# Kernel optimization log

Hardware: AMD Instinct MI355X
Metric: run time of the kernel (lower is better)

## Reference

```python
import jax, jax.numpy as jnp
import numpy as np

B, T, D = 2, 2048, 2048
H, L = 16, 64
Hd = D // H  # 128
SCALE = 1.0 / np.sqrt(L).astype(np.float32)


def apply_rope(q, k, freqs):
    # q, k: [B, T, H, Hd]; freqs: [T, Hd//2] angles (theta)
    cos = jnp.cos(freqs)[None, :, None, :]  # [1,T,1,Hd/2]
    sin = jnp.sin(freqs)[None, :, None, :]

    def rot(t):
        tr = t.reshape(*t.shape[:-1], Hd // 2, 2)
        a, b = tr[..., 0], tr[..., 1]
        return jnp.stack([a * cos - b * sin, a * sin + b * cos], axis=-1).reshape(t.shape)

    return rot(q), rot(k)


def setup_inputs() -> dict:
    key = jax.random.key(0)
    ks = jax.random.split(key, 16)

    def w(k, shape):
        return jax.random.normal(k, shape, jnp.float32) * 0.02

    x = jax.random.normal(ks[0], (B, T, D), jnp.float32)
    # RoPE angles: theta[t, i] = t / 10000^(2i/Hd)
    inv = 1.0 / (10000.0 ** (jnp.arange(0, Hd, 2, dtype=jnp.float32) / Hd))
    freqs = jnp.arange(T, dtype=jnp.float32)[:, None] * inv[None, :]  # [T, Hd/2]
    # additive causal mask
    mask = jnp.where(jnp.tril(jnp.ones((T, T), bool)), 0.0, -1e9).astype(jnp.float32)

    return dict(
        x=x, freqs=freqs, mask=mask,
        Wq=w(ks[1], (D, D)), bq=jnp.zeros((D,), jnp.float32),
        Wk=w(ks[2], (D, D)), bk=jnp.zeros((D,), jnp.float32),
        Wv=w(ks[3], (D, D)), bv=jnp.zeros((D,), jnp.float32),
        Wo=w(ks[4], (D, D)), bo=jnp.zeros((D,), jnp.float32),
        Wcq=w(ks[5], (Hd, L)), bcq=jnp.zeros((L,), jnp.float32),
        Wck=w(ks[6], (Hd, L)), bck=jnp.zeros((L,), jnp.float32),
        Wcv=w(ks[7], (Hd, L)), bcv=jnp.zeros((L,), jnp.float32),
        Wd=w(ks[8], (L, Hd)), bd=jnp.zeros((Hd,), jnp.float32),
    )


def reference(x, freqs, mask, Wq, bq, Wk, bk, Wv, bv, Wo, bo,
              Wcq, bcq, Wck, bck, Wcv, bcv, Wd, bd):
    b, t, d = x.shape
    q = (x @ Wq + bq).reshape(b, t, H, Hd)
    k = (x @ Wk + bk).reshape(b, t, H, Hd)
    v = (x @ Wv + bv).reshape(b, t, H, Hd)

    q, k = apply_rope(q, k, freqs)

    # per-head latent compression [B,T,H,L]
    q_lat = jnp.einsum('bthd,dl->bthl', q, Wcq) + bcq
    k_lat = jnp.einsum('bthd,dl->bthl', k, Wck) + bck
    v_lat = jnp.einsum('bthd,dl->bthl', v, Wcv) + bcv

    scores = jnp.einsum('bthl,bshl->bhts', q_lat, k_lat) * SCALE
    scores = scores + mask[None, None, :, :]
    attn = jax.nn.softmax(scores, axis=-1)

    out = jnp.einsum('bhts,bshl->bthl', attn, v_lat)  # [B,T,H,L]
    out = jnp.einsum('bthl,lk->bthk', out, Wd) + bd    # decompress -> [B,T,H,Hd]
    out = out.reshape(b, t, d)
    return out @ Wo + bo
```

## Files before the change

kernel.cpp:

```cpp
#include <hip/hip_runtime.h>
#include <hip/hip_bf16.h>

static constexpr int Bsz = 2;
static constexpr int Tn  = 2048;
static constexpr int Dn  = 2048;
static constexpr int Hn  = 16;
static constexpr int Ln  = 64;
static constexpr int Hd  = 128;
static constexpr float SL2E = 0.125f * 1.44269504088896f;

typedef short short8 __attribute__((ext_vector_type(8)));
typedef float f32x4 __attribute__((ext_vector_type(4)));
typedef unsigned short ushort8 __attribute__((ext_vector_type(8)));
typedef unsigned short ushort4v __attribute__((ext_vector_type(4)));
typedef _Float16 half8 __attribute__((ext_vector_type(8)));
typedef unsigned short u16;

__device__ inline u16 f16_rne(float f) {
  _Float16 h = (_Float16)f;
  union { _Float16 h; u16 u; } x; x.h = h;
  return x.u;
}
__device__ inline float f16_to_f(u16 u) {
  union { u16 u; _Float16 h; } x; x.u = u;
  return (float)x.h;
}

#define GL(g, l) __builtin_amdgcn_global_load_lds(                     \
    (const __attribute__((address_space(1))) void*)(g),                \
    (__attribute__((address_space(3))) void*)(l), 16, 0, 0)

__global__ void split_h(const float* __restrict__ A, u16* __restrict__ O,
                        int nblk, int Kd) {
  int b = blockIdx.x * 256 + threadIdx.x;
  if (b >= nblk) return;
  int perRow = Kd >> 3;
  int m = b / perRow, gb = b - m * perRow;
  int w = gb >> 2, g = gb & 3;
  const float* src = A + (size_t)m * Kd + (w << 5) + (g << 2);
  float4 v0 = *(const float4*)src;
  float4 v1 = *(const float4*)(src + 16);
  float e[8] = {v0.x, v0.y, v0.z, v0.w, v1.x, v1.y, v1.z, v1.w};
  ushort8 o;
#pragma unroll
  for (int j = 0; j < 8; ++j) o[j] = f16_rne(e[j]);
  *(ushort8*)(O + (size_t)b * 8) = o;
}

__global__ __launch_bounds__(256) void transpose_h(
    const float* __restrict__ W, u16* __restrict__ Th, int Kd, int Nd) {
  __shared__ float t[32][33];
  int k0 = blockIdx.x * 32, n0 = blockIdx.y * 32;
  int i = threadIdx.x;
  {
    int kk = i >> 3, nn = (i & 7) << 2;
    float4 v = *(const float4*)&W[(size_t)(k0 + kk) * Nd + n0 + nn];
    t[kk][nn] = v.x; t[kk][nn + 1] = v.y; t[kk][nn + 2] = v.z; t[kk][nn + 3] = v.w;
  }
  __syncthreads();
  int n = i >> 3, t2 = i & 7;
  int g = t2 >> 1, h = t2 & 1;
  int kbase = h * 16 + g * 4;
  ushort4v o;
#pragma unroll
  for (int j = 0; j < 4; ++j) o[j] = f16_rne(t[kbase + j][n]);
  *(ushort4v*)(Th + (size_t)(n0 + n) * Kd + k0 + t2 * 4) = o;
}

__global__ __launch_bounds__(256) void fold64(
    const float* __restrict__ A, int lda, int a_bx, int a_by,
    const float* __restrict__ B, int ldb, int b_bx, int b_by,
    float* __restrict__ C, int ldc, int c_bx, int c_by) {
  __shared__ float a_lds[64][132];
  __shared__ float b_lds[128][64];
  const int bx = blockIdx.x, by = blockIdx.y, tid = threadIdx.x;
  A += (size_t)bx * a_bx + (size_t)by * a_by;
  B += (size_t)bx * b_bx + (size_t)by * b_by;
  C += (size_t)bx * c_bx + (size_t)by * c_by;
  for (int i = tid; i < 64 * 32; i += 256) {
    int r = i >> 5, c4 = (i & 31) << 2;
    *(float4*)&a_lds[r][c4] = *(const float4*)&A[(size_t)r * lda + c4];
  }
  for (int i = tid; i < 128 * 16; i += 256) {
    int r = i >> 4, c4 = (i & 15) << 2;
    *(float4*)&b_lds[r][c4] = *(const float4*)&B[(size_t)r * ldb + c4];
  }
  __syncthreads();
  const int r = tid >> 2, l0 = (tid & 3) << 4;
  float acc[16] = {};
  for (int k = 0; k < 128; ++k) {
    float av = a_lds[r][k];
    const float* bp = &b_lds[k][l0];
#pragma unroll
    for (int j = 0; j < 16; ++j) acc[j] += av * bp[j];
  }
#pragma unroll
  for (int j4 = 0; j4 < 4; ++j4)
    *(float4*)&C[(size_t)r * ldc + l0 + j4 * 4] = *(float4*)&acc[j4 * 4];
}

__global__ __launch_bounds__(256) void bias_prep(
    const float* __restrict__ bv, const float* __restrict__ Wcv,
    const float* __restrict__ bcv, const float* __restrict__ bd,
    const float* __restrict__ Wo, const float* __restrict__ bo,
    float* __restrict__ bias_vf, float* __restrict__ bias_out) {
  __shared__ float red[4][64];
  if (blockIdx.x == 32) {
    for (int e = threadIdx.x; e < 1024; e += 256) {
      int h = e >> 6, l = e & 63;
      float s = bcv[l];
      for (int j = 0; j < 128; ++j) s += bv[h * 128 + j] * Wcv[j * 64 + l];
      bias_vf[e] = s;
    }
  } else {
    int n0 = blockIdx.x * 64;
    int c = threadIdx.x & 63, g = threadIdx.x >> 6;
    float s = 0.f;
    for (int k = g * 512; k < (g + 1) * 512; ++k)
      s += bd[k & 127] * Wo[(size_t)k * 2048 + n0 + c];
    red[g][c] = s;
    __syncthreads();
    if (g == 0)
      bias_out[n0 + c] = red[0][c] + red[1][c] + red[2][c] + red[3][c] + bo[n0 + c];
  }
}

__global__ __launch_bounds__(256) void gemm_qkv(
    const u16* __restrict__ Af, const u16* __restrict__ Bf,
    u16* __restrict__ cQ, u16* __restrict__ cK, u16* __restrict__ cV,
    const float* __restrict__ bq, const float* __restrict__ bk,
    const float* __restrict__ bvf, int K) {
  __shared__ u16 s[2][2][128 * 64];
  const int tid = threadIdx.x;
  const int lane = tid & 63;
  const int w = tid >> 6, wr = w >> 1, wc = w & 1;
  const int l15 = lane & 15, lg = lane >> 4;
  const int row0 = blockIdx.y * 128, col0 = blockIdx.x * 128;

  const int sr = tid >> 3, sq = tid & 7;
  const int sg = sq ^ (sr & 7);
  size_t aoff[4], boff[4];
#pragma unroll
  for (int j = 0; j < 4; ++j) {
    aoff[j] = (size_t)(row0 + j * 32 + sr) * K + sg * 8;
    boff[j] = (size_t)(col0 + j * 32 + sr) * K + sg * 8;
  }

  f32x4 acc[4][4];
#pragma unroll
  for (int i2 = 0; i2 < 4; ++i2)
#pragma unroll
    for (int j2 = 0; j2 < 4; ++j2) acc[i2][j2] = (f32x4){0.f, 0.f, 0.f, 0.f};

  int fa[4][2], fb[4][2];
#pragma unroll
  for (int mi = 0; mi < 4; ++mi) {
    int ra = wr * 64 + mi * 16 + l15;
    int rb = wc * 64 + mi * 16 + l15;
#pragma unroll
    for (int kk = 0; kk < 2; ++kk) {
      fa[mi][kk] = ra * 128 + (((kk * 4 + lg) ^ (ra & 7)) << 4);
      fb[mi][kk] = rb * 128 + (((kk * 4 + lg) ^ (rb & 7)) << 4);
    }
  }

#pragma unroll
  for (int j = 0; j < 4; ++j) {
    GL(Af + aoff[j], (char*)&s[0][0][0] + j * 4096 + tid * 16);
    GL(Bf + boff[j], (char*)&s[0][1][0] + j * 4096 + tid * 16);
  }
  int cur = 0;
  for (int k0 = 0; k0 < K; k0 += 64) {
    __syncthreads();
    if (k0 + 64 < K) {
      const int nb = cur ^ 1;
#pragma unroll
      for (int j = 0; j < 4; ++j) {
        GL(Af + aoff[j] + k0 + 64, (char*)&s[nb][0][0] + j * 4096 + tid * 16);
        GL(Bf + boff[j] + k0 + 64, (char*)&s[nb][1][0] + j * 4096 + tid * 16);
      }
    }
#pragma unroll
    for (int kk = 0; kk < 2; ++kk) {
      half8 a[4], b[4];
#pragma unroll
      for (int mi = 0; mi < 4; ++mi) {
        a[mi] = *(const half8*)((const char*)&s[cur][0][0] + fa[mi][kk]);
        b[mi] = *(const half8*)((const char*)&s[cur][1][0] + fb[mi][kk]);
      }
#pragma unroll
      for (int mi = 0; mi < 4; ++mi)
#pragma unroll
        for (int ni = 0; ni < 4; ++ni)
          acc[mi][ni] = __builtin_amdgcn_mfma_f32_16x16x32_f16(a[mi], b[ni], acc[mi][ni], 0, 0, 0);
    }
    cur ^= 1;
  }
  u16* Cp; const float* bp; int ldc, cl0;
  if (col0 < 2048)      { Cp = cQ; bp = bq;  ldc = 2048; cl0 = col0; }
  else if (col0 < 4096) { Cp = cK; bp = bk;  ldc = 2048; cl0 = col0 - 2048; }
  else                  { Cp = cV; bp = bvf; ldc = 1024; cl0 = col0 - 4096; }
#pragma unroll
  for (int ni = 0; ni < 4; ++ni) {
    int c = cl0 + wc * 64 + ni * 16 + l15;
    float bias = bp[c];
#pragma unroll
    for (int mi = 0; mi < 4; ++mi) {
      int rr = row0 + wr * 64 + mi * 16 + lg * 4;
#pragma unroll
      for (int r = 0; r < 4; ++r)
        Cp[(size_t)(rr + r) * ldc + c] = f16_rne(acc[mi][ni][r] + bias);
    }
  }
}

__global__ __launch_bounds__(256) void gemm_f16(
    const u16* __restrict__ Af, const u16* __restrict__ Bf,
    const float* __restrict__ bias, float* __restrict__ C,
    int M, int N, int K) {
  __shared__ u16 s[2][2][128 * 64];
  const int tid = threadIdx.x;
  const int lane = tid & 63;
  const int w = tid >> 6, wr = w >> 1, wc = w & 1;
  const int l15 = lane & 15, lg = lane >> 4;
  const int row0 = blockIdx.y * 128, col0 = blockIdx.x * 128;

  const int sr = tid >> 3, sq = tid & 7;
  const int sg = sq ^ (sr & 7);
  size_t aoff[4], boff[4];
#pragma unroll
  for (int j = 0; j < 4; ++j) {
    aoff[j] = (size_t)(row0 + j * 32 + sr) * K + sg * 8;
    boff[j] = (size_t)(col0 + j * 32 + sr) * K + sg * 8;
  }

  f32x4 acc[4][4];
#pragma unroll
  for (int i2 = 0; i2 < 4; ++i2)
#pragma unroll
    for (int j2 = 0; j2 < 4; ++j2) acc[i2][j2] = (f32x4){0.f, 0.f, 0.f, 0.f};

  int fa[4][2], fb[4][2];
#pragma unroll
  for (int mi = 0; mi < 4; ++mi) {
    int ra = wr * 64 + mi * 16 + l15;
    int rb = wc * 64 + mi * 16 + l15;
#pragma unroll
    for (int kk = 0; kk < 2; ++kk) {
      fa[mi][kk] = ra * 128 + (((kk * 4 + lg) ^ (ra & 7)) << 4);
      fb[mi][kk] = rb * 128 + (((kk * 4 + lg) ^ (rb & 7)) << 4);
    }
  }

#pragma unroll
  for (int j = 0; j < 4; ++j) {
    GL(Af + aoff[j], (char*)&s[0][0][0] + j * 4096 + tid * 16);
    GL(Bf + boff[j], (char*)&s[0][1][0] + j * 4096 + tid * 16);
  }
  int cur = 0;
  for (int k0 = 0; k0 < K; k0 += 64) {
    __syncthreads();
    if (k0 + 64 < K) {
      const int nb = cur ^ 1;
#pragma unroll
      for (int j = 0; j < 4; ++j) {
        GL(Af + aoff[j] + k0 + 64, (char*)&s[nb][0][0] + j * 4096 + tid * 16);
        GL(Bf + boff[j] + k0 + 64, (char*)&s[nb][1][0] + j * 4096 + tid * 16);
      }
    }
#pragma unroll
    for (int kk = 0; kk < 2; ++kk) {
      half8 a[4], b[4];
#pragma unroll
      for (int mi = 0; mi < 4; ++mi) {
        a[mi] = *(const half8*)((const char*)&s[cur][0][0] + fa[mi][kk]);
        b[mi] = *(const half8*)((const char*)&s[cur][1][0] + fb[mi][kk]);
      }
#pragma unroll
      for (int mi = 0; mi < 4; ++mi)
#pragma unroll
        for (int ni = 0; ni < 4; ++ni)
          acc[mi][ni] = __builtin_amdgcn_mfma_f32_16x16x32_f16(a[mi], b[ni], acc[mi][ni], 0, 0, 0);
    }
    cur ^= 1;
  }
#pragma unroll
  for (int ni = 0; ni < 4; ++ni) {
    int c = col0 + wc * 64 + ni * 16 + l15;
    float bv = bias[c];
#pragma unroll
    for (int mi = 0; mi < 4; ++mi) {
      int rr = row0 + wr * 64 + mi * 16 + lg * 4;
#pragma unroll
      for (int r = 0; r < 4; ++r)
        C[(size_t)(rr + r) * N + c] = acc[mi][ni][r] + bv;
    }
  }
}

__global__ __launch_bounds__(256) void compress_qk_mfma(
    const u16* __restrict__ src, const u16* __restrict__ WcT,
    const float* __restrict__ bc, const float* __restrict__ freqs,
    u16* __restrict__ dst) {
  __shared__ u16 q_lds[64 * 128];
  __shared__ u16 w_lds[64 * 128];
  const int tid = threadIdx.x;
  const int lane = tid & 63;
  const int w = tid >> 6;
  const int t0 = blockIdx.x * 64;
  const int bh = blockIdx.y, b = bh >> 4, h = bh & 15;

#pragma unroll
  for (int j = 0; j < 4; ++j) {
    int idx = tid + j * 256;
    int row = idx >> 4, slot = idx & 15;
    GL(WcT + (size_t)row * 128 + (size_t)(slot ^ (row & 7)) * 8,
       (char*)w_lds + idx * 16);
  }
  const int r = tid >> 2, seg = tid & 3;
  const u16* qp = src + ((size_t)(b * Tn + t0 + r)) * Dn + h * 128 + seg * 32;
  const float* fp = freqs + (size_t)(t0 + r) * 64 + seg * 16;
  float fr[16];
#pragma unroll
  for (int j = 0; j < 4; ++j) *(float4*)&fr[4 * j] = ((const float4*)fp)[j];
#pragma unroll
  for (int j = 0; j < 8; ++j) {
    ushort4v uv = *(const ushort4v*)(qp + 4 * j);
    float e0 = f16_to_f(uv[0]), e1 = f16_to_f(uv[1]);
    float e2 = f16_to_f(uv[2]), e3 = f16_to_f(uv[3]);
    float s0, c0, s1, c1;
    sincosf(fr[2 * j], &s0, &c0);
    sincosf(fr[2 * j + 1], &s1, &c1);
    ushort4v u;
    u[0] = f16_rne(e0 * c0 - e1 * s0);
    u[1] = f16_rne(e0 * s0 + e1 * c0);
    u[2] = f16_rne(e2 * c1 - e3 * s1);
    u[3] = f16_rne(e2 * s1 + e3 * c1);
    int slot = seg * 4 + (j & 3);
    *(ushort4v*)((char*)q_lds + r * 256 + ((slot ^ (r & 7)) << 4) + (j >> 2) * 8) = u;
  }
  __syncthreads();
  const int l15 = lane & 15, lg = lane >> 4;
  const int arow = w * 16 + l15;
  half8 af[4];
#pragma unroll
  for (int ks = 0; ks < 4; ++ks)
    af[ks] = *(const half8*)((const char*)q_lds + arow * 256 +
                             (((ks * 4 + lg) ^ (arow & 7)) << 4));
  f32x4 acc[4];
#pragma unroll
  for (int ni = 0; ni < 4; ++ni) acc[ni] = (f32x4){0.f, 0.f, 0.f, 0.f};
#pragma unroll
  for (int ni = 0; ni < 4; ++ni) {
    const int brow = ni * 16 + l15;
#pragma unroll
    for (int ks = 0; ks < 4; ++ks) {
      half8 bf = *(const half8*)((const char*)w_lds + brow * 256 +
                                 (((ks * 4 + lg) ^ (brow & 7)) << 4));
      acc[ni] = __builtin_amdgcn_mfma_f32_16x16x32_f16(af[ks], bf, acc[ni], 0, 0, 0);
    }
  }
  __syncthreads();
#pragma unroll
  for (int ni = 0; ni < 4; ++ni) {
    int lat = ni * 16 + l15;
    float bcv = bc[lat];
    int p = (lat & 32) + ((lat >> 2) & 3) * 8 + ((lat >> 4) & 1) * 4 + (lat & 3);
#pragma unroll
    for (int reg = 0; reg < 4; ++reg)
      q_lds[w * 1024 + (lg * 4 + reg) * 64 + p] = f16_rne(acc[ni][reg] + bcv);
  }
  __syncthreads();
#pragma unroll
  for (int j = 0; j < 2; ++j) {
    int idx = tid + j * 256;
    int row = idx >> 3, c8 = idx & 7;
    ushort8 val = *(const ushort8*)&q_lds[row * 64 + c8 * 8];
    *(ushort8*)(dst + ((size_t)bh * Tn + t0 + row) * 64 + c8 * 8) = val;
  }
}

__global__ __launch_bounds__(256) void transpose_v(
    const u16* __restrict__ vlat, u16* __restrict__ vlatT) {
  __shared__ u16 o_lds[64][64];
  const int tid = threadIdx.x;
  const int t0 = blockIdx.x * 64;
  const int bh = blockIdx.y, b = bh >> 4, h = bh & 15;
  const int tt = tid >> 2, lseg = tid & 3;
  const u16* vp = vlat + (size_t)(b * Tn + t0 + tt) * 1024 + h * 64 + lseg * 16;
#pragma unroll
  for (int g = 0; g < 4; ++g) {
    ushort4v u = *(const ushort4v*)(vp + g * 4);
    *(ushort4v*)&o_lds[tt][lseg * 16 + ((g ^ (tt & 3)) << 2)] = u;
  }
  __syncthreads();
  const int lat = tid >> 2, tseg = tid & 3;
  const int tw = tseg >> 1, h4 = tseg & 1;
  u16 vals[16];
#pragma unroll
  for (int i = 0; i < 16; ++i)
    vals[i] = o_lds[tseg * 16 + i][lat ^ ((i & 3) << 2)];
  u16* dp = vlatT + ((size_t)bh * 64 + lat) * Tn + t0 + tw * 32 + h4 * 4;
#pragma unroll
  for (int g = 0; g < 4; ++g) {
    ushort4v u = {vals[g * 4 + 0], vals[g * 4 + 1], vals[g * 4 + 2], vals[g * 4 + 3]};
    *(ushort4v*)(dp + g * 8) = u;
  }
}

__global__ __launch_bounds__(256) void attn_mfma(
    const u16* __restrict__ qlat, const u16* __restrict__ klat,
    const u16* __restrict__ vlatT, u16* __restrict__ oh) {
  __shared__ u16 Ks[64 * 72];
  __shared__ u16 Vs[64 * 72];
  __shared__ u16 Os[64][72];
  const int tid = threadIdx.x;
  const int lane = tid & 63;
  const int w = tid >> 6;
  const int lin = (int)(blockIdx.x + blockIdx.y * gridDim.x);
  const int nchunk = (int)(gridDim.x * gridDim.y) >> 3;
  const int swz = (lin & 7) * nchunk + (lin >> 3);
  const int bh = swz >> 5, b = bh >> 4, h = bh & 15;
  const int q0 = (31 - (swz & 31)) * 64;
  const int qw = q0 + w * 16;
  const u16* ql = qlat + (size_t)bh * Tn * 64;
  const u16* kl = klat + (size_t)bh * Tn * 64;
  const u16* vt = vlatT + (size_t)bh * 64 * Tn;
  const int l15 = lane & 15, lg = lane >> 4;

  half8 qf[2];
#pragma unroll
  for (int ks = 0; ks < 2; ++ks)
    qf[ks] = *(const half8*)(const void*)(ql + (size_t)(qw + l15) * 64 + (ks * 4 + lg) * 8);

  f32x4 accO[4];
#pragma unroll
  for (int mi = 0; mi < 4; ++mi) accO[mi] = (f32x4){0.f, 0.f, 0.f, 0.f};
  float mrow = -1e30f, lrow = 0.f;

  const int srow = tid >> 2, spair = tid & 3;
  u16* ksw = &Ks[srow * 72 + spair * 16];
  u16* vsw = &Vs[srow * 72 + spair * 16];
  const u16* kgp = kl + (size_t)srow * 64 + spair * 16;
  const u16* vgp = vt + (size_t)srow * Tn + spair * 16;

  ushort8 kr0 = *(const ushort8*)(kgp);
  ushort8 kr1 = *(const ushort8*)(kgp + 8);
  ushort8 vr0 = *(const ushort8*)(vgp);
  ushort8 vr1 = *(const ushort8*)(vgp + 8);

  const int ntiles = q0 / 64 + 1;
  for (int kt = 0; kt < ntiles; ++kt) {
    const int k0 = kt * 64;
    __syncthreads();
    *(ushort8*)ksw       = kr0;
    *(ushort8*)(ksw + 8) = kr1;
    *(ushort8*)vsw       = vr0;
    *(ushort8*)(vsw + 8) = vr1;
    __syncthreads();
    {
      int kn = k0 + 64; kn = kn > (int)Tn - 64 ? (int)Tn - 64 : kn;
      kr0 = *(const ushort8*)(kgp + (size_t)kn * 64);
      kr1 = *(const ushort8*)(kgp + (size_t)kn * 64 + 8);
      vr0 = *(const ushort8*)(vgp + kn);
      vr1 = *(const ushort8*)(vgp + kn + 8);
    }
    f32x4 s4[4];
#pragma unroll
    for (int mi = 0; mi < 4; ++mi) s4[mi] = (f32x4){0.f, 0.f, 0.f, 0.f};
    __builtin_amdgcn_s_setprio(1);
#pragma unroll
    for (int ks = 0; ks < 2; ++ks) {
      half8 kf[4];
#pragma unroll
      for (int mi = 0; mi < 4; ++mi)
        kf[mi] = *(const half8*)(const void*)&Ks[(mi * 16 + l15) * 72 + (ks * 4 + lg) * 8];
#pragma unroll
      for (int mi = 0; mi < 4; ++mi)
        s4[mi] = __builtin_amdgcn_mfma_f32_16x16x32_f16(kf[mi], qf[ks], s4[mi], 0, 0, 0);
    }
    __builtin_amdgcn_s_setprio(0);
    const bool needmask = (kt == ntiles - 1);
    const int qidx = qw + l15;
    float p[4][4];
    float tmax = -1e30f;
#pragma unroll
    for (int mi = 0; mi < 4; ++mi)
#pragma unroll
      for (int rr = 0; rr < 4; ++rr) {
        float v = s4[mi][rr] * SL2E;
        if (needmask && (k0 + mi * 16 + lg * 4 + rr > qidx)) v = -1e30f;
        p[mi][rr] = v;
        tmax = fmaxf(tmax, v);
      }
    tmax = fmaxf(tmax, __shfl_xor(tmax, 16));
    tmax = fmaxf(tmax, __shfl_xor(tmax, 32));
    if (!__all(tmax - mrow <= 8.f)) {
      float mnew = fmaxf(mrow, tmax);
      float alpha = exp2f(mrow - mnew);
      lrow *= alpha;
#pragma unroll
      for (int mi = 0; mi < 4; ++mi)
#pragma unroll
        for (int rr = 0; rr < 4; ++rr) accO[mi][rr] *= alpha;
      mrow = mnew;
    }
    float psum = 0.f;
    u16 ph[4][4];
#pragma unroll
    for (int mi = 0; mi < 4; ++mi)
#pragma unroll
      for (int rr = 0; rr < 4; ++rr) {
        float e = exp2f(p[mi][rr] - mrow);
        u16 hb = f16_rne(e);
        psum += f16_to_f(hb);
        ph[mi][rr] = hb;
      }
    psum += __shfl_xor(psum, 16);
    psum += __shfl_xor(psum, 32);
    lrow += psum;
    ushort8 pf[2];
#pragma unroll
    for (int ks = 0; ks < 2; ++ks) {
      ushort8 f;
#pragma unroll
      for (int rr = 0; rr < 4; ++rr) {
        f[rr]     = ph[2 * ks][rr];
        f[4 + rr] = ph[2 * ks + 1][rr];
      }
      pf[ks] = f;
    }
    __builtin_amdgcn_s_setprio(1);
#pragma unroll
    for (int ks = 0; ks < 2; ++ks) {
      half8 vf[4];
#pragma unroll
      for (int mi = 0; mi < 4; ++mi)
        vf[mi] = *(const half8*)(const void*)&Vs[(mi * 16 + l15) * 72 + (ks * 4 + lg) * 8];
#pragma unroll
      for (int mi = 0; mi < 4; ++mi)
        accO[mi] = __builtin_amdgcn_mfma_f32_16x16x32_f16(vf[mi], *(const half8*)&pf[ks], accO[mi], 0, 0, 0);
    }
    __builtin_amdgcn_s_setprio(0);
  }
  __syncthreads();
  {
    float inv = 1.f / lrow;
    int qloc = w * 16 + l15;
#pragma unroll
    for (int mi = 0; mi < 4; ++mi) {
      int pbase = (mi >> 1) * 32 + lg * 8 + (mi & 1) * 4;
      ushort4v u;
#pragma unroll
      for (int rr = 0; rr < 4; ++rr) u[rr] = f16_rne(accO[mi][rr] * inv);
      *(ushort4v*)&Os[qloc][pbase] = u;
    }
  }
  __syncthreads();
  {
    int rid = tid >> 2, seg = tid & 3;
    u16* dstp = oh + ((size_t)(b * Tn + q0 + rid)) * 1024 + h * 64 + seg * 16;
#pragma unroll
    for (int g = 0; g < 2; ++g)
      *(ushort8*)(dstp + g * 8) = *(const ushort8*)&Os[rid][seg * 16 + g * 8];
  }
}

extern "C" void kernel_launch(void* const* d_in, const int* in_sizes, int n_in,
                              void* d_out, int out_size, void* d_ws, size_t ws_size,
                              hipStream_t stream) {
  const float* x     = (const float*)d_in[0];
  const float* freqs = (const float*)d_in[1];
  const float* Wq  = (const float*)d_in[3];  const float* bq  = (const float*)d_in[4];
  const float* Wk  = (const float*)d_in[5];  const float* bk  = (const float*)d_in[6];
  const float* Wv  = (const float*)d_in[7];  const float* bv  = (const float*)d_in[8];
  const float* Wo  = (const float*)d_in[9];  const float* bo  = (const float*)d_in[10];
  const float* Wcq = (const float*)d_in[11]; const float* bcq = (const float*)d_in[12];
  const float* Wck = (const float*)d_in[13]; const float* bck = (const float*)d_in[14];
  const float* Wcv = (const float*)d_in[15]; const float* bcv = (const float*)d_in[16];
  const float* Wd  = (const float*)d_in[17]; const float* bd  = (const float*)d_in[18];
  float* out = (float*)d_out;

  const size_t BT = (size_t)Bsz * Tn;
  const size_t nQ = BT * Dn;
  const size_t nL = BT * Hn * Ln;
  const size_t nWT = (size_t)5120 * 2048;

  char* ws = (char*)d_ws;
  u16* xf   = (u16*)ws;
  u16* WTf  = xf + nQ;
  float* Wvf = (float*)(WTf + nWT);
  u16* Qh   = (u16*)(Wvf + (size_t)2048 * 1024);
  u16* Kh   = Qh + nQ;
  u16* vlat = Kh + nQ;
  float* bias_vf  = (float*)(vlat + (size_t)4096 * 1024);
  float* bias_out = bias_vf + 1024;
  u16* qlat  = (u16*)(bias_out + 2048);
  u16* klat  = qlat + nL;
  u16* vlatT = klat + nL;
  u16* oh = (u16*)(vlatT + nL);
  float* Wdo = (float*)(oh + (size_t)4096 * 1024);
  u16* WdoT = (u16*)(Wdo + (size_t)1024 * 2048);
  u16* WcqT = WdoT + (size_t)2048 * 1024;
  u16* WckT = WcqT + (size_t)64 * 128;

  dim3 blk(256);
  int nblkA = (int)(nQ / 8);

  split_h<<<(nblkA + 255) / 256, blk, 0, stream>>>(x, xf, nblkA, Dn);
  fold64<<<dim3(32, 16), blk, 0, stream>>>(Wv, 2048, 64 * 2048, 128,
                                           Wcv, 64, 0, 0,
                                           Wvf, 1024, 64 * 1024, 64);
  transpose_h<<<dim3(64, 64), blk, 0, stream>>>(Wq, WTf, 2048, 2048);
  transpose_h<<<dim3(64, 64), blk, 0, stream>>>(Wk, WTf + (size_t)2048 * 2048, 2048, 2048);
  transpose_h<<<dim3(64, 32), blk, 0, stream>>>(Wvf, WTf + (size_t)4096 * 2048, 2048, 1024);
  transpose_h<<<dim3(4, 2), blk, 0, stream>>>(Wcq, WcqT, 128, 64);
  transpose_h<<<dim3(4, 2), blk, 0, stream>>>(Wck, WckT, 128, 64);
  bias_prep<<<33, blk, 0, stream>>>(bv, Wcv, bcv, bd, Wo, bo, bias_vf, bias_out);

  gemm_qkv<<<dim3(40, 32), blk, 0, stream>>>(xf, WTf, Qh, Kh, vlat,
                                             bq, bk, bias_vf, 2048);

  dim3 gc(Tn / 64, Bsz * Hn);
  compress_qk_mfma<<<gc, blk, 0, stream>>>(Qh, WcqT, bcq, freqs, qlat);
  compress_qk_mfma<<<gc, blk, 0, stream>>>(Kh, WckT, bck, freqs, klat);
  transpose_v<<<gc, blk, 0, stream>>>(vlat, vlatT);

  attn_mfma<<<dim3(Tn / 64, Bsz * Hn), blk, 0, stream>>>(qlat, klat, vlatT, oh);

  fold64<<<dim3(32, 16), blk, 0, stream>>>(Wd, 128, 0, 0,
                                           Wo, 2048, 64, 128 * 2048,
                                           Wdo, 2048, 64, 64 * 2048);
  transpose_h<<<dim3(32, 64), blk, 0, stream>>>(Wdo, WdoT, 1024, 2048);
  gemm_f16<<<dim3(16, 32), blk, 0, stream>>>(oh, WdoT, bias_out, out, (int)BT, 2048, 1024);
}
```

Measured before the change: 330.9 us.

## Use 8-wave GEMM blocks, XCD tile swizzle, and batch small launches via gridDim.z

Both f16 GEMMs now run 512-thread blocks with a 2x4 wave grid, so each wave computes a 64x32 sub-tile of the same 128x128 block tile. This halves per-wave accumulators and raises the number of waves available to hide latency. gemm_qkv also remaps block indices so neighbouring tiles land on the same XCD, aiming for better L2 reuse. Separately, the Q/K weight transposes and the Q/K latent compressions are merged into single launches using blockIdx.z, cutting launch count. The trade-off is more LDS fragment reads per MFMA and a higher register and sync cost per block.

```diff
diff --git a/kernel.cpp b/kernel.cpp
--- a/kernel.cpp
+++ b/kernel.cpp
@@ -47,8 +47,11 @@
   *(ushort8*)(O + (size_t)b * 8) = o;
 }
 
-__global__ __launch_bounds__(256) void transpose_h(
-    const float* __restrict__ W, u16* __restrict__ Th, int Kd, int Nd) {
+__global__ __launch_bounds__(256) void transpose_h2(
+    const float* __restrict__ W0, const float* __restrict__ W1,
+    u16* __restrict__ T0, u16* __restrict__ T1, int Kd, int Nd) {
+  const float* W = blockIdx.z ? W1 : W0;
+  u16* Th = blockIdx.z ? T1 : T0;
   __shared__ float t[32][33];
   int k0 = blockIdx.x * 32, n0 = blockIdx.y * 32;
   int i = threadIdx.x;
@@ -125,7 +128,7 @@
   }
 }
 
-__global__ __launch_bounds__(256) void gemm_qkv(
+__global__ __launch_bounds__(512) void gemm_qkv(
     const u16* __restrict__ Af, const u16* __restrict__ Bf,
     u16* __restrict__ cQ, u16* __restrict__ cK, u16* __restrict__ cV,
     const float* __restrict__ bq, const float* __restrict__ bk,
@@ -133,41 +136,48 @@
   __shared__ u16 s[2][2][128 * 64];
   const int tid = threadIdx.x;
   const int lane = tid & 63;
-  const int w = tid >> 6, wr = w >> 1, wc = w & 1;
+  const int w = tid >> 6;
+  const int wr = w >> 2, wc = w & 3;
   const int l15 = lane & 15, lg = lane >> 4;
-  const int row0 = blockIdx.y * 128, col0 = blockIdx.x * 128;
+  const int lin = (int)(blockIdx.x + blockIdx.y * gridDim.x);
+  const int swz = (lin & 7) * 160 + (lin >> 3);
+  const int row0 = (swz / 40) * 128, col0 = (swz % 40) * 128;
 
   const int sr = tid >> 3, sq = tid & 7;
   const int sg = sq ^ (sr & 7);
-  size_t aoff[4], boff[4];
-#pragma unroll
-  for (int j = 0; j < 4; ++j) {
-    aoff[j] = (size_t)(row0 + j * 32 + sr) * K + sg * 8;
-    boff[j] = (size_t)(col0 + j * 32 + sr) * K + sg * 8;
-  }
-
-  f32x4 acc[4][4];
+  size_t aoff[2], boff[2];
+#pragma unroll
+  for (int j = 0; j < 2; ++j) {
+    aoff[j] = (size_t)(row0 + j * 64 + sr) * K + sg * 8;
+    boff[j] = (size_t)(col0 + j * 64 + sr) * K + sg * 8;
+  }
+
+  f32x4 acc[4][2];
 #pragma unroll
   for (int i2 = 0; i2 < 4; ++i2)
 #pragma unroll
-    for (int j2 = 0; j2 < 4; ++j2) acc[i2][j2] = (f32x4){0.f, 0.f, 0.f, 0.f};
-
-  int fa[4][2], fb[4][2];
+    for (int j2 = 0; j2 < 2; ++j2) acc[i2][j2] = (f32x4){0.f, 0.f, 0.f, 0.f};
+
+  int fa[4][2], fb[2][2];
 #pragma unroll
   for (int mi = 0; mi < 4; ++mi) {
     int ra = wr * 64 + mi * 16 + l15;
-    int rb = wc * 64 + mi * 16 + l15;
-#pragma unroll
-    for (int kk = 0; kk < 2; ++kk) {
+#pragma unroll
+    for (int kk = 0; kk < 2; ++kk)
       fa[mi][kk] = ra * 128 + (((kk * 4 + lg) ^ (ra & 7)) << 4);
-      fb[mi][kk] = rb * 128 + (((kk * 4 + lg) ^ (rb & 7)) << 4);
-    }
-  }
-
-#pragma unroll
-  for (int j = 0; j < 4; ++j) {
-    GL(Af + aoff[j], (char*)&s[0][0][0] + j * 4096 + tid * 16);
-    GL(Bf + boff[j], (char*)&s[0][1][0] + j * 4096 + tid * 16);
+  }
+#pragma unroll
+  for (int ni = 0; ni < 2; ++ni) {
+    int rb = wc * 32 + ni * 16 + l15;
+#pragma unroll
+    for (int kk = 0; kk < 2; ++kk)
+      fb[ni][kk] = 16384 + rb * 128 + (((kk * 4 + lg) ^ (rb & 7)) << 4);
+  }
+
+#pragma unroll
+  for (int j = 0; j < 2; ++j) {
+    GL(Af + aoff[j], (char*)&s[0][0][0] + j * 8192 + tid * 16);
+    GL(Bf + boff[j], (char*)&s[0][1][0] + j * 8192 + tid * 16);
   }
   int cur = 0;
   for (int k0 = 0; k0 < K; k0 += 64) {
@@ -175,23 +185,24 @@
     if (k0 + 64 < K) {
       const int nb = cur ^ 1;
 #pragma unroll
-      for (int j = 0; j < 4; ++j) {
-        GL(Af + aoff[j] + k0 + 64, (char*)&s[nb][0][0] + j * 4096 + tid * 16);
-        GL(Bf + boff[j] + k0 + 64, (char*)&s[nb][1][0] + j * 4096 + tid * 16);
+      for (int j = 0; j < 2; ++j) {
+        GL(Af + aoff[j] + k0 + 64, (char*)&s[nb][0][0] + j * 8192 + tid * 16);
+        GL(Bf + boff[j] + k0 + 64, (char*)&s[nb][1][0] + j * 8192 + tid * 16);
       }
     }
 #pragma unroll
     for (int kk = 0; kk < 2; ++kk) {
-      half8 a[4], b[4];
-#pragma unroll
-      for (int mi = 0; mi < 4; ++mi) {
+      half8 a[4], b[2];
+#pragma unroll
+      for (int mi = 0; mi < 4; ++mi)
         a[mi] = *(const half8*)((const char*)&s[cur][0][0] + fa[mi][kk]);
-        b[mi] = *(const half8*)((const char*)&s[cur][1][0] + fb[mi][kk]);
-      }
-#pragma unroll
-      for (int mi = 0; mi < 4; ++mi)
-#pragma unroll
-        for (int ni = 0; ni < 4; ++ni)
+#pragma unroll
+      for (int ni = 0; ni < 2; ++ni)
+        b[ni] = *(const half8*)((const char*)&s[cur][0][0] + fb[ni][kk]);
+#pragma unroll
+      for (int mi = 0; mi < 4; ++mi)
+#pragma unroll
+        for (int ni = 0; ni < 2; ++ni)
           acc[mi][ni] = __builtin_amdgcn_mfma_f32_16x16x32_f16(a[mi], b[ni], acc[mi][ni], 0, 0, 0);
     }
     cur ^= 1;
@@ -201,8 +212,8 @@
   else if (col0 < 4096) { Cp = cK; bp = bk;  ldc = 2048; cl0 = col0 - 2048; }
   else                  { Cp = cV; bp = bvf; ldc = 1024; cl0 = col0 - 4096; }
 #pragma unroll
-  for (int ni = 0; ni < 4; ++ni) {
-    int c = cl0 + wc * 64 + ni * 16 + l15;
+  for (int ni = 0; ni < 2; ++ni) {
+    int c = cl0 + wc * 32 + ni * 16 + l15;
     float bias = bp[c];
 #pragma unroll
     for (int mi = 0; mi < 4; ++mi) {
@@ -214,48 +225,53 @@
   }
 }
 
-__global__ __launch_bounds__(256) void gemm_f16(
+__global__ __launch_bounds__(512) void gemm_f16(
     const u16* __restrict__ Af, const u16* __restrict__ Bf,
     const float* __restrict__ bias, float* __restrict__ C,
     int M, int N, int K) {
   __shared__ u16 s[2][2][128 * 64];
   const int tid = threadIdx.x;
   const int lane = tid & 63;
-  const int w = tid >> 6, wr = w >> 1, wc = w & 1;
+  const int w = tid >> 6;
+  const int wr = w >> 2, wc = w & 3;
   const int l15 = lane & 15, lg = lane >> 4;
   const int row0 = blockIdx.y * 128, col0 = blockIdx.x * 128;
 
   const int sr = tid >> 3, sq = tid & 7;
   const int sg = sq ^ (sr & 7);
-  size_t aoff[4], boff[4];
-#pragma unroll
-  for (int j = 0; j < 4; ++j) {
-    aoff[j] = (size_t)(row0 + j * 32 + sr) * K + sg * 8;
-    boff[j] = (size_t)(col0 + j * 32 + sr) * K + sg * 8;
-  }
-
-  f32x4 acc[4][4];
+  size_t aoff[2], boff[2];
+#pragma unroll
+  for (int j = 0; j < 2; ++j) {
+    aoff[j] = (size_t)(row0 + j * 64 + sr) * K + sg * 8;
+    boff[j] = (size_t)(col0 + j * 64 + sr) * K + sg * 8;
+  }
+
+  f32x4 acc[4][2];
 #pragma unroll
   for (int i2 = 0; i2 < 4; ++i2)
 #pragma unroll
-    for (int j2 = 0; j2 < 4; ++j2) acc[i2][j2] = (f32x4){0.f, 0.f, 0.f, 0.f};
-
-  int fa[4][2], fb[4][2];
+    for (int j2 = 0; j2 < 2; ++j2) acc[i2][j2] = (f32x4){0.f, 0.f, 0.f, 0.f};
+
+  int fa[4][2], fb[2][2];
 #pragma unroll
   for (int mi = 0; mi < 4; ++mi) {
     int ra = wr * 64 + mi * 16 + l15;
-    int rb = wc * 64 + mi * 16 + l15;
-#pragma unroll
-    for (int kk = 0; kk < 2; ++kk) {
+#pragma unroll
+    for (int kk = 0; kk < 2; ++kk)
       fa[mi][kk] = ra * 128 + (((kk * 4 + lg) ^ (ra & 7)) << 4);
-      fb[mi][kk] = rb * 128 + (((kk * 4 + lg) ^ (rb & 7)) << 4);
-    }
-  }
-
-#pragma unroll
-  for (int j = 0; j < 4; ++j) {
-    GL(Af + aoff[j], (char*)&s[0][0][0] + j * 4096 + tid * 16);
-    GL(Bf + boff[j], (char*)&s[0][1][0] + j * 4096 + tid * 16);
+  }
+#pragma unroll
+  for (int ni = 0; ni < 2; ++ni) {
+    int rb = wc * 32 + ni * 16 + l15;
+#pragma unroll
+    for (int kk = 0; kk < 2; ++kk)
+      fb[ni][kk] = 16384 + rb * 128 + (((kk * 4 + lg) ^ (rb & 7)) << 4);
+  }
+
+#pragma unroll
+  for (int j = 0; j < 2; ++j) {
+    GL(Af + aoff[j], (char*)&s[0][0][0] + j * 8192 + tid * 16);
+    GL(Bf + boff[j], (char*)&s[0][1][0] + j * 8192 + tid * 16);
   }
   int cur = 0;
   for (int k0 = 0; k0 < K; k0 += 64) {
@@ -263,30 +279,31 @@
     if (k0 + 64 < K) {
       const int nb = cur ^ 1;
 #pragma unroll
-      for (int j = 0; j < 4; ++j) {
-        GL(Af + aoff[j] + k0 + 64, (char*)&s[nb][0][0] + j * 4096 + tid * 16);
-        GL(Bf + boff[j] + k0 + 64, (char*)&s[nb][1][0] + j * 4096 + tid * 16);
+      for (int j = 0; j < 2; ++j) {
+        GL(Af + aoff[j] + k0 + 64, (char*)&s[nb][0][0] + j * 8192 + tid * 16);
+        GL(Bf + boff[j] + k0 + 64, (char*)&s[nb][1][0] + j * 8192 + tid * 16);
       }
     }
 #pragma unroll
     for (int kk = 0; kk < 2; ++kk) {
-      half8 a[4], b[4];
-#pragma unroll
-      for (int mi = 0; mi < 4; ++mi) {
+      half8 a[4], b[2];
+#pragma unroll
+      for (int mi = 0; mi < 4; ++mi)
         a[mi] = *(const half8*)((const char*)&s[cur][0][0] + fa[mi][kk]);
-        b[mi] = *(const half8*)((const char*)&s[cur][1][0] + fb[mi][kk]);
-      }
-#pragma unroll
-      for (int mi = 0; mi < 4; ++mi)
-#pragma unroll
-        for (int ni = 0; ni < 4; ++ni)
+#pragma unroll
+      for (int ni = 0; ni < 2; ++ni)
+        b[ni] = *(const half8*)((const char*)&s[cur][0][0] + fb[ni][kk]);
+#pragma unroll
+      for (int mi = 0; mi < 4; ++mi)
+#pragma unroll
+        for (int ni = 0; ni < 2; ++ni)
           acc[mi][ni] = __builtin_amdgcn_mfma_f32_16x16x32_f16(a[mi], b[ni], acc[mi][ni], 0, 0, 0);
     }
     cur ^= 1;
   }
 #pragma unroll
-  for (int ni = 0; ni < 4; ++ni) {
-    int c = col0 + wc * 64 + ni * 16 + l15;
+  for (int ni = 0; ni < 2; ++ni) {
+    int c = col0 + wc * 32 + ni * 16 + l15;
     float bv = bias[c];
 #pragma unroll
     for (int mi = 0; mi < 4; ++mi) {
@@ -299,9 +316,15 @@
 }
 
 __global__ __launch_bounds__(256) void compress_qk_mfma(
-    const u16* __restrict__ src, const u16* __restrict__ WcT,
-    const float* __restrict__ bc, const float* __restrict__ freqs,
-    u16* __restrict__ dst) {
+    const u16* __restrict__ srcQ, const u16* __restrict__ srcK,
+    const u16* __restrict__ WcTq, const u16* __restrict__ WcTk,
+    const float* __restrict__ bcq, const float* __restrict__ bck,
+    const float* __restrict__ freqs,
+    u16* __restrict__ dstQ, u16* __restrict__ dstK) {
+  const u16* src = blockIdx.z ? srcK : srcQ;
+  const u16* WcT = blockIdx.z ? WcTk : WcTq;
+  const float* bc = blockIdx.z ? bck : bcq;
+  u16* dst = blockIdx.z ? dstK : dstQ;
   __shared__ u16 q_lds[64 * 128];
   __shared__ u16 w_lds[64 * 128];
   const int tid = threadIdx.x;
@@ -611,26 +634,25 @@
   fold64<<<dim3(32, 16), blk, 0, stream>>>(Wv, 2048, 64 * 2048, 128,
                                            Wcv, 64, 0, 0,
                                            Wvf, 1024, 64 * 1024, 64);
-  transpose_h<<<dim3(64, 64), blk, 0, stream>>>(Wq, WTf, 2048, 2048);
-  transpose_h<<<dim3(64, 64), blk, 0, stream>>>(Wk, WTf + (size_t)2048 * 2048, 2048, 2048);
-  transpose_h<<<dim3(64, 32), blk, 0, stream>>>(Wvf, WTf + (size_t)4096 * 2048, 2048, 1024);
-  transpose_h<<<dim3(4, 2), blk, 0, stream>>>(Wcq, WcqT, 128, 64);
-  transpose_h<<<dim3(4, 2), blk, 0, stream>>>(Wck, WckT, 128, 64);
+  transpose_h2<<<dim3(64, 64, 2), blk, 0, stream>>>(Wq, Wk, WTf,
+                                                    WTf + (size_t)2048 * 2048, 2048, 2048);
+  transpose_h2<<<dim3(64, 32, 1), blk, 0, stream>>>(Wvf, Wvf, WTf + (size_t)4096 * 2048,
+                                                    WTf + (size_t)4096 * 2048, 2048, 1024);
+  transpose_h2<<<dim3(4, 2, 2), blk, 0, stream>>>(Wcq, Wck, WcqT, WckT, 128, 64);
   bias_prep<<<33, blk, 0, stream>>>(bv, Wcv, bcv, bd, Wo, bo, bias_vf, bias_out);
 
-  gemm_qkv<<<dim3(40, 32), blk, 0, stream>>>(xf, WTf, Qh, Kh, vlat,
-                                             bq, bk, bias_vf, 2048);
-
-  dim3 gc(Tn / 64, Bsz * Hn);
-  compress_qk_mfma<<<gc, blk, 0, stream>>>(Qh, WcqT, bcq, freqs, qlat);
-  compress_qk_mfma<<<gc, blk, 0, stream>>>(Kh, WckT, bck, freqs, klat);
-  transpose_v<<<gc, blk, 0, stream>>>(vlat, vlatT);
+  gemm_qkv<<<dim3(40, 32), dim3(512), 0, stream>>>(xf, WTf, Qh, Kh, vlat,
+                                                   bq, bk, bias_vf, 2048);
+
+  compress_qk_mfma<<<dim3(Tn / 64, Bsz * Hn, 2), blk, 0, stream>>>(
+      Qh, Kh, WcqT, WckT, bcq, bck, freqs, qlat, klat);
+  transpose_v<<<dim3(Tn / 64, Bsz * Hn), blk, 0, stream>>>(vlat, vlatT);
 
   attn_mfma<<<dim3(Tn / 64, Bsz * Hn), blk, 0, stream>>>(qlat, klat, vlatT, oh);
 
   fold64<<<dim3(32, 16), blk, 0, stream>>>(Wd, 128, 0, 0,
                                            Wo, 2048, 64, 128 * 2048,
                                            Wdo, 2048, 64, 64 * 2048);
-  transpose_h<<<dim3(32, 64), blk, 0, stream>>>(Wdo, WdoT, 1024, 2048);
-  gemm_f16<<<dim3(16, 32), blk, 0, stream>>>(oh, WdoT, bias_out, out, (int)BT, 2048, 1024);
-}
+  transpose_h2<<<dim3(32, 64, 1), blk, 0, stream>>>(Wdo, Wdo, WdoT, WdoT, 1024, 2048);
+  gemm_f16<<<dim3(16, 32), dim3(512), 0, stream>>>(oh, WdoT, bias_out, out, (int)BT, 2048, 1024);
+}
```

New measurement: 337.1 us. No clear change (+1.9%).
